# Kernel optimization log

Hardware: AMD Instinct MI355X
Metric: run time of the kernel (lower is better)

Reference implementation:

```python
import jax, jax.numpy as jnp
import numpy as np

B, T, IN, H = 32, 256, 64, 128
TOP_K = 5
TRUNC = 100   # truncate_length: detach h,c every TRUNC steps
EPS = 1e-7
NEG = -1e9


def setup_inputs() -> dict:
    key = jax.random.key(0)
    ks = jax.random.split(key, 6)
    s = 1.0 / np.sqrt(H)  # torch LSTMCell default init bound
    xav = float(1.414 * np.sqrt(6.0 / (2 * H + 1)))  # xavier_uniform gain=1.414
    return {
        "x": jax.random.normal(ks[0], (B, T, IN), jnp.float32),
        "W_ih": jax.random.uniform(ks[1], (4 * H, IN), jnp.float32, -s, s),
        "W_hh": jax.random.uniform(ks[2], (4 * H, H), jnp.float32, -s, s),
        "b_ih": jax.random.uniform(ks[3], (4 * H,), jnp.float32, -s, s),
        "b_hh": jax.random.uniform(ks[4], (4 * H,), jnp.float32, -s, s),
        "w_t": jax.random.uniform(ks[5], (2 * H, 1), jnp.float32, -xav, xav),
    }


def _lstm_cell(x_t, h, c, W_ih, W_hh, b_ih, b_hh):
    # torch gate order: i, f, g, o
    g = x_t @ W_ih.T + h @ W_hh.T + (b_ih + b_hh)
    i, f, gg, o = jnp.split(g, 4, axis=-1)
    c = jax.nn.sigmoid(f) * c + jax.nn.sigmoid(i) * jnp.tanh(gg)
    h = jax.nn.sigmoid(o) * jnp.tanh(c)
    return h, c


def reference(x, W_ih, W_hh, b_ih, b_hh, w_t):
    Bv, Tv, _ = x.shape
    Hh = W_hh.shape[1]
    # score = w_t . tanh(cat(h_t, h_old)) splits additively since tanh is elementwise
    w_a = w_t[:Hh, 0]
    w_b = w_t[Hh:, 0]
    pos = jnp.arange(Tv + 1)

    def step(carry, inp):
        h, c, h_old = carry          # h_old: [B, T+1, H], slot 0 = initial zeros
        i, x_t = inp
        det = ((i + 1) % TRUNC) == 0
        h = jnp.where(det, jax.lax.stop_gradient(h), h)
        c = jnp.where(det, jax.lax.stop_gradient(c), c)
        h, c = _lstm_cell(x_t, h, c, W_ih, W_hh, b_ih, b_hh)
        rem = i + 1                  # remember_size
        mask = pos < rem             # [T+1] valid memory slots
        # attention scores over stored states
        s = (jnp.tanh(h) @ w_a)[:, None] + jnp.tanh(h_old) @ w_b  # [B, T+1]
        s_valid = jnp.where(mask[None, :], s, NEG)
        delta = jax.lax.top_k(s_valid, TOP_K)[0][:, -1] + EPS
        w_sp = jnp.clip(s_valid - delta[:, None], 0.0)
        w_sp = w_sp / (w_sp.sum(axis=1, keepdims=True) + EPS)
        # Sparse_attention returns raw scores when remember_size <= top_k
        attn_w = jnp.where(rem <= TOP_K, s, w_sp)
        attn_c = jnp.einsum('bt,bth->bh', jnp.where(mask[None, :], attn_w, 0.0), h_old)
        h = h + attn_c
        h_old = jax.lax.dynamic_update_slice(h_old, h[:, None, :], (0, rem, 0))
        return (h, c, h_old), (attn_c, attn_w)

    h0 = jnp.zeros((Bv, Hh), x.dtype)
    c0 = jnp.zeros((Bv, Hh), x.dtype)
    buf0 = jnp.zeros((Bv, Tv + 1, Hh), x.dtype)
    xs = (jnp.arange(Tv), jnp.swapaxes(x, 0, 1))
    _, (attn_c_all, attn_w_all) = jax.lax.scan(step, (h0, c0, buf0), xs)
    # module returns last step's (attn_c, out_attn_w); final remember_size == T
    return attn_c_all[-1], attn_w_all[-1][:, :Tv, None]
```

## Files before the change

### kernel.cpp

```cpp
#include <hip/hip_runtime.h>
#include <math.h>

#define NEGF -1000000000.0f
#define EPSF 1e-7f


#define RAWBAR() asm volatile("s_waitcnt lgkmcnt(0)\n\ts_barrier" ::: "memory")

__device__ __forceinline__ float fsigmoid(float x) {
  return 1.0f / (1.0f + __expf(-x));
}
__device__ __forceinline__ float ftanh(float x) {
  return 1.0f - 2.0f / (1.0f + __expf(2.0f * x));
}

__device__ __forceinline__ float wave_allsum(float v) {
#if __has_builtin(__builtin_amdgcn_update_dpp) && __has_builtin(__builtin_amdgcn_readlane)
  float f = v;
#define DPPSTEP(ctrl, rmask) { \
    int t = __builtin_amdgcn_update_dpp(0, __builtin_bit_cast(int, f), \
                                        ctrl, rmask, 0xf, true); \
    f += __builtin_bit_cast(float, t); }
  DPPSTEP(0x111, 0xf)
  DPPSTEP(0x112, 0xf)
  DPPSTEP(0x114, 0xf)
  DPPSTEP(0x118, 0xf)
  DPPSTEP(0x142, 0xa)
  DPPSTEP(0x143, 0x8)
#undef DPPSTEP
  return __builtin_bit_cast(float,
      __builtin_amdgcn_readlane(__builtin_bit_cast(int, f), 63));
#else
  for (int off = 1; off < 64; off <<= 1) v += __shfl_xor(v, off, 64);
  return v;
#endif
}

__global__ __launch_bounds__(512) void xw_kernel(
    const float* __restrict__ x, const float* __restrict__ W_ih,
    const float* __restrict__ b_ih, const float* __restrict__ b_hh,
    float* __restrict__ xw)
{
  const int t0 = blockIdx.x * 32;
  const int b  = blockIdx.y;
  const int g  = threadIdx.x;

  __shared__ float sx[32 * 64];
  ((float4*)sx)[threadIdx.x] =
      ((const float4*)(x + (size_t)(b * 256 + t0) * 64))[threadIdx.x];

  const float4* wr = (const float4*)(W_ih + (size_t)g * 64);
  float4 w0 = wr[0],  w1 = wr[1],  w2 = wr[2],  w3 = wr[3],
         w4 = wr[4],  w5 = wr[5],  w6 = wr[6],  w7 = wr[7],
         w8 = wr[8],  w9 = wr[9],  w10 = wr[10], w11 = wr[11],
         w12 = wr[12], w13 = wr[13], w14 = wr[14], w15 = wr[15];
  const float bias = b_ih[g] + b_hh[g];
  __syncthreads();

  float* dst = xw + (size_t)(b * 256 + t0) * 512 + g;
  for (int tt = 0; tt < 32; ++tt) {
    const float4* xr = (const float4*)(sx + tt * 64);
    float a0 = 0.0f, a1 = 0.0f, a2 = 0.0f, a3 = 0.0f;
#define XSTEP(j) { float4 hv = xr[j]; \
    a0 = fmaf(w##j.x, hv.x, a0); a1 = fmaf(w##j.y, hv.y, a1); \
    a2 = fmaf(w##j.z, hv.z, a2); a3 = fmaf(w##j.w, hv.w, a3); }
    XSTEP(0) XSTEP(1) XSTEP(2) XSTEP(3) XSTEP(4) XSTEP(5) XSTEP(6) XSTEP(7)
    XSTEP(8) XSTEP(9) XSTEP(10) XSTEP(11) XSTEP(12) XSTEP(13) XSTEP(14) XSTEP(15)
#undef XSTEP
    dst[(size_t)tt * 512] = (a0 + a1) + (a2 + a3) + bias;
  }
}

__global__
__attribute__((amdgpu_flat_work_group_size(512, 512), amdgpu_waves_per_eu(2, 2)))
void lstm_attn(
    const float* __restrict__ xw, const float* __restrict__ W_hh,
    const float* __restrict__ w_t, float* __restrict__ out)
{
  const int b   = blockIdx.x;
  const int tid = threadIdx.x;
  const int l   = tid & 63;
  const int wid = tid >> 6;
  const int p   = tid & 127;
  const int q   = tid >> 7;

  __shared__ float ho[257 * 128];
  __shared__ float sh_part[4 * 512];
  __shared__ float sh_d[8];

  const float4* pI = (const float4*)(W_hh + (size_t)(p      ) * 128 + (q << 5));
  const float4* pF = (const float4*)(W_hh + (size_t)(p + 128) * 128 + (q << 5));
  const float4* pG = (const float4*)(W_hh + (size_t)(p + 256) * 128 + (q << 5));
  const float4* pO = (const float4*)(W_hh + (size_t)(p + 384) * 128 + (q << 5));
  float4 wI0 = pI[0], wI1 = pI[1], wI2 = pI[2], wI3 = pI[3],
         wI4 = pI[4], wI5 = pI[5], wI6 = pI[6], wI7 = pI[7];
  float4 wF0 = pF[0], wF1 = pF[1], wF2 = pF[2], wF3 = pF[3],
         wF4 = pF[4], wF5 = pF[5], wF6 = pF[6], wF7 = pF[7];
  float4 wG0 = pG[0], wG1 = pG[1], wG2 = pG[2], wG3 = pG[3],
         wG4 = pG[4], wG5 = pG[5], wG6 = pG[6], wG7 = pG[7];
  float4 wO0 = pO[0], wO1 = pO[1], wO2 = pO[2], wO3 = pO[3],
         wO4 = pO[4], wO5 = pO[5], wO6 = pO[6], wO7 = pO[7];

  const int j0 = 2 * l, j1 = 2 * l + 1;
  float c0 = 0.0f, c1 = 0.0f;
  float wa0 = 0.0f, wa1 = 0.0f, wb0 = 0.0f, wb1 = 0.0f;
  float t5v0 = 0.0f, t5v1 = NEGF, t5v2 = NEGF, t5v3 = NEGF, t5v4 = NEGF;
  int   t5i0 = 0, t5i1 = 0, t5i2 = 0, t5i3 = 0;
  float gn0 = 0.0f, gn1 = 0.0f, gn2 = 0.0f, gn3 = 0.0f;
  int   ofs0 = 0, ofs1 = 0, ofs2 = 0, ofs3 = 0;

  if (wid == 0) {
    wa0 = w_t[j0];       wa1 = w_t[j1];
    wb0 = w_t[128 + j0]; wb1 = w_t[128 + j1];
    *(float2*)(ho + j0) = make_float2(0.0f, 0.0f);
    __builtin_amdgcn_s_setprio(1);
  }
  if (tid == 0) sh_d[0] = 0.0f;
  __syncthreads();

  const float* xwb = xw + (size_t)b * 256 * 512;
  float xcI = 0.0f, xcF = 0.0f, xcG = 0.0f, xcO = 0.0f;
  if (q == 0) {
    xcI = xwb[p];       xcF = xwb[p + 128];
    xcG = xwb[p + 256]; xcO = xwb[p + 384];
  }

  for (int i = 0; i < 256; ++i) {
    const int rem = i + 1;
    float hn0 = 0.0f, hn1 = 0.0f;

    float aI = xcI, aF = xcF, aG = xcG, aO = xcO;
    if (q == 0 && i < 255) {
      const float* xn = xwb + (size_t)(i + 1) * 512;
      xcI = xn[p];       xcF = xn[p + 128];
      xcG = xn[p + 256]; xcO = xn[p + 384];
    }
    const float4* hh4 = (const float4*)(ho + i * 128 + (q << 5));
#define KS(k) { float4 hv = hh4[k]; \
    aI = fmaf(wI##k.x, hv.x, aI); aI = fmaf(wI##k.y, hv.y, aI); \
    aI = fmaf(wI##k.z, hv.z, aI); aI = fmaf(wI##k.w, hv.w, aI); \
    aF = fmaf(wF##k.x, hv.x, aF); aF = fmaf(wF##k.y, hv.y, aF); \
    aF = fmaf(wF##k.z, hv.z, aF); aF = fmaf(wF##k.w, hv.w, aF); \
    aG = fmaf(wG##k.x, hv.x, aG); aG = fmaf(wG##k.y, hv.y, aG); \
    aG = fmaf(wG##k.z, hv.z, aG); aG = fmaf(wG##k.w, hv.w, aG); \
    aO = fmaf(wO##k.x, hv.x, aO); aO = fmaf(wO##k.y, hv.y, aO); \
    aO = fmaf(wO##k.z, hv.z, aO); aO = fmaf(wO##k.w, hv.w, aO); }
    KS(0) KS(1) KS(2) KS(3) KS(4) KS(5) KS(6) KS(7)
#undef KS
    {
      float* sp = sh_part + (q << 9) + p;
      sp[0]   = aI;
      sp[128] = aF;
      sp[256] = aG;
      sp[384] = aO;
    }

    float2 hv0, hv1, hv2, hv3;
    if (wid == 0 && i >= 5) {
      hv0 = *(const float2*)(ho + ofs0);
      hv1 = *(const float2*)(ho + ofs1);
      hv2 = *(const float2*)(ho + ofs2);
      hv3 = *(const float2*)(ho + ofs3);
    }
    RAWBAR();

    if (wid == 0) {
#define GSUM(base) ({ \
      float2 x0 = ((const float2*)(sh_part        + (base)))[l]; \
      float2 x1 = ((const float2*)(sh_part +  512 + (base)))[l]; \
      float2 x2 = ((const float2*)(sh_part + 1024 + (base)))[l]; \
      float2 x3 = ((const float2*)(sh_part + 1536 + (base)))[l]; \
      float2 r; r.x = (x0.x + x1.x) + (x2.x + x3.x); \
      r.y = (x0.y + x1.y) + (x2.y + x3.y); r; })
      float2 Pi = GSUM(0), Pf = GSUM(128), Pg = GSUM(256), Po = GSUM(384);
#undef GSUM
      c0 = fsigmoid(Pf.x) * c0 + fsigmoid(Pi.x) * ftanh(Pg.x);
      c1 = fsigmoid(Pf.y) * c1 + fsigmoid(Pi.y) * ftanh(Pg.y);
      float hc0 = fsigmoid(Po.x) * ftanh(c0);
      float hc1 = fsigmoid(Po.y) * ftanh(c1);

      float at0, at1;
      if (i >= 5) {
        at0 = gn0 * hv0.x;            at1 = gn0 * hv0.y;
        at0 = fmaf(gn1, hv1.x, at0);  at1 = fmaf(gn1, hv1.y, at1);
        at0 = fmaf(gn2, hv2.x, at0);  at1 = fmaf(gn2, hv2.y, at1);
        at0 = fmaf(gn3, hv3.x, at0);  at1 = fmaf(gn3, hv3.y, at1);
      } else {
        float a = wave_allsum(ftanh(hc0) * wa0 + ftanh(hc1) * wa1);
        at0 = 0.0f; at1 = 0.0f;
        for (int t = 0; t <= i; ++t) {
          float s = a + sh_d[t];
          float2 hv = *(const float2*)(ho + t * 128 + j0);
          at0 = fmaf(s, hv.x, at0);
          at1 = fmaf(s, hv.y, at1);
        }
      }
      hn0 = hc0 + at0; hn1 = hc1 + at1;
      *(float2*)(ho + rem * 128 + j0) = make_float2(hn0, hn1);
      if (i == 255) {
        out[b * 128 + j0] = at0; out[b * 128 + j1] = at1;
        #pragma unroll
        for (int m = 0; m < 4; ++m) {
          int t = l + 64 * m;
          float val = 0.0f;
          if (t == t5i0) val = gn0;
          if (t == t5i1) val = gn1;
          if (t == t5i2) val = gn2;
          if (t == t5i3) val = gn3;
          out[4096 + b * 256 + t] = val;
        }
      }
    }
    RAWBAR();

    if (wid == 0 && i < 255) {
      float dn = wave_allsum(ftanh(hn0) * wb0 + ftanh(hn1) * wb1);
      if (l == 0 && i < 4) sh_d[rem] = dn;
      float v = dn; int vi = rem;
      if (v > t5v0) { float tv = t5v0; int ti = t5i0; t5v0 = v; t5i0 = vi; v = tv; vi = ti; }
      if (v > t5v1) { float tv = t5v1; int ti = t5i1; t5v1 = v; t5i1 = vi; v = tv; vi = ti; }
      if (v > t5v2) { float tv = t5v2; int ti = t5i2; t5v2 = v; t5i2 = vi; v = tv; vi = ti; }
      if (v > t5v3) { float tv = t5v3; int ti = t5i3; t5v3 = v; t5i3 = vi; v = tv; vi = ti; }
      if (v > t5v4) { t5v4 = v; }
      float g0 = fmaxf(t5v0 - t5v4 - EPSF, 0.0f);
      float g1 = fmaxf(t5v1 - t5v4 - EPSF, 0.0f);
      float g2 = fmaxf(t5v2 - t5v4 - EPSF, 0.0f);
      float g3 = fmaxf(t5v3 - t5v4 - EPSF, 0.0f);
      float inv = 1.0f / (((g0 + g1) + (g2 + g3)) + EPSF);
      gn0 = g0 * inv; gn1 = g1 * inv; gn2 = g2 * inv; gn3 = g3 * inv;
      ofs0 = (t5i0 << 7) + j0; ofs1 = (t5i1 << 7) + j0;
      ofs2 = (t5i2 << 7) + j0; ofs3 = (t5i3 << 7) + j0;
    }
  }
}

extern "C" void kernel_launch(void* const* d_in, const int* in_sizes, int n_in,
                              void* d_out, int out_size, void* d_ws, size_t ws_size,
                              hipStream_t stream) {
  const float* x    = (const float*)d_in[0];
  const float* W_ih = (const float*)d_in[1];
  const float* W_hh = (const float*)d_in[2];
  const float* b_ih = (const float*)d_in[3];
  const float* b_hh = (const float*)d_in[4];
  const float* w_t  = (const float*)d_in[5];
  float* out = (float*)d_out;

  float* xw = (float*)d_ws;

  xw_kernel<<<dim3(8, 32), 512, 0, stream>>>(x, W_ih, b_ih, b_hh, xw);
  lstm_attn<<<dim3(32), 512, 0, stream>>>(xw, W_hh, w_t, out);
}
```

Before: 398.1 us.

## Fuse input projection into recurrent LSTM kernel with prefetched x ring buffer

Removes the separate xw_kernel and its workspace round trip. The recurrent kernel now keeps W_ih slices in registers and computes the x·W_ih^T contribution each step from a small shared-memory ring of x rows. Wave 7 prefetches those rows several steps ahead. This saves a kernel launch and the global reads of the precomputed projection, but adds 64 FMAs per gate per thread and more register pressure to the serial per-step critical path.

Result: slower. 487.6 us (+22.5%).

```diff
diff --git a/kernel.cpp b/kernel.cpp
--- a/kernel.cpp
+++ b/kernel.cpp
@@ -36,46 +36,13 @@
 #endif
 }
 
-__global__ __launch_bounds__(512) void xw_kernel(
-    const float* __restrict__ x, const float* __restrict__ W_ih,
-    const float* __restrict__ b_ih, const float* __restrict__ b_hh,
-    float* __restrict__ xw)
-{
-  const int t0 = blockIdx.x * 32;
-  const int b  = blockIdx.y;
-  const int g  = threadIdx.x;
-
-  __shared__ float sx[32 * 64];
-  ((float4*)sx)[threadIdx.x] =
-      ((const float4*)(x + (size_t)(b * 256 + t0) * 64))[threadIdx.x];
-
-  const float4* wr = (const float4*)(W_ih + (size_t)g * 64);
-  float4 w0 = wr[0],  w1 = wr[1],  w2 = wr[2],  w3 = wr[3],
-         w4 = wr[4],  w5 = wr[5],  w6 = wr[6],  w7 = wr[7],
-         w8 = wr[8],  w9 = wr[9],  w10 = wr[10], w11 = wr[11],
-         w12 = wr[12], w13 = wr[13], w14 = wr[14], w15 = wr[15];
-  const float bias = b_ih[g] + b_hh[g];
-  __syncthreads();
-
-  float* dst = xw + (size_t)(b * 256 + t0) * 512 + g;
-  for (int tt = 0; tt < 32; ++tt) {
-    const float4* xr = (const float4*)(sx + tt * 64);
-    float a0 = 0.0f, a1 = 0.0f, a2 = 0.0f, a3 = 0.0f;
-#define XSTEP(j) { float4 hv = xr[j]; \
-    a0 = fmaf(w##j.x, hv.x, a0); a1 = fmaf(w##j.y, hv.y, a1); \
-    a2 = fmaf(w##j.z, hv.z, a2); a3 = fmaf(w##j.w, hv.w, a3); }
-    XSTEP(0) XSTEP(1) XSTEP(2) XSTEP(3) XSTEP(4) XSTEP(5) XSTEP(6) XSTEP(7)
-    XSTEP(8) XSTEP(9) XSTEP(10) XSTEP(11) XSTEP(12) XSTEP(13) XSTEP(14) XSTEP(15)
-#undef XSTEP
-    dst[(size_t)tt * 512] = (a0 + a1) + (a2 + a3) + bias;
-  }
-}
-
 __global__
 __attribute__((amdgpu_flat_work_group_size(512, 512), amdgpu_waves_per_eu(2, 2)))
 void lstm_attn(
-    const float* __restrict__ xw, const float* __restrict__ W_hh,
-    const float* __restrict__ w_t, float* __restrict__ out)
+    const float* __restrict__ x, const float* __restrict__ W_ih,
+    const float* __restrict__ W_hh, const float* __restrict__ b_ih,
+    const float* __restrict__ b_hh, const float* __restrict__ w_t,
+    float* __restrict__ out)
 {
   const int b   = blockIdx.x;
   const int tid = threadIdx.x;
@@ -86,6 +53,7 @@
 
   __shared__ float ho[257 * 128];
   __shared__ float sh_part[4 * 512];
+  __shared__ float sxr[8][64];
   __shared__ float sh_d[8];
 
   const float4* pI = (const float4*)(W_hh + (size_t)(p      ) * 128 + (q << 5));
@@ -100,6 +68,20 @@
          wG4 = pG[4], wG5 = pG[5], wG6 = pG[6], wG7 = pG[7];
   float4 wO0 = pO[0], wO1 = pO[1], wO2 = pO[2], wO3 = pO[3],
          wO4 = pO[4], wO5 = pO[5], wO6 = pO[6], wO7 = pO[7];
+  const float4* xI = (const float4*)(W_ih + (size_t)(p      ) * 64 + (q << 4));
+  const float4* xF = (const float4*)(W_ih + (size_t)(p + 128) * 64 + (q << 4));
+  const float4* xG = (const float4*)(W_ih + (size_t)(p + 256) * 64 + (q << 4));
+  const float4* xO = (const float4*)(W_ih + (size_t)(p + 384) * 64 + (q << 4));
+  float4 vI0 = xI[0], vI1 = xI[1], vI2 = xI[2], vI3 = xI[3];
+  float4 vF0 = xF[0], vF1 = xF[1], vF2 = xF[2], vF3 = xF[3];
+  float4 vG0 = xG[0], vG1 = xG[1], vG2 = xG[2], vG3 = xG[3];
+  float4 vO0 = xO[0], vO1 = xO[1], vO2 = xO[2], vO3 = xO[3];
+  const float biasI = (q == 0) ? b_ih[p      ] + b_hh[p      ] : 0.0f;
+  const float biasF = (q == 0) ? b_ih[p + 128] + b_hh[p + 128] : 0.0f;
+  const float biasG = (q == 0) ? b_ih[p + 256] + b_hh[p + 256] : 0.0f;
+  const float biasO = (q == 0) ? b_ih[p + 384] + b_hh[p + 384] : 0.0f;
+
+  const float* xg = x + (size_t)b * 256 * 64;
 
   const int j0 = 2 * l, j1 = 2 * l + 1;
   float c0 = 0.0f, c1 = 0.0f;
@@ -115,26 +97,36 @@
     *(float2*)(ho + j0) = make_float2(0.0f, 0.0f);
     __builtin_amdgcn_s_setprio(1);
   }
+  if (wid == 7) {
+    sxr[0][l] = xg[l];
+    sxr[1][l] = xg[64 + l];
+    sxr[2][l] = xg[128 + l];
+    sxr[3][l] = xg[192 + l];
+    sxr[4][l] = xg[256 + l];
+  }
   if (tid == 0) sh_d[0] = 0.0f;
   __syncthreads();
-
-  const float* xwb = xw + (size_t)b * 256 * 512;
-  float xcI = 0.0f, xcF = 0.0f, xcG = 0.0f, xcO = 0.0f;
-  if (q == 0) {
-    xcI = xwb[p];       xcF = xwb[p + 128];
-    xcG = xwb[p + 256]; xcO = xwb[p + 384];
-  }
 
   for (int i = 0; i < 256; ++i) {
     const int rem = i + 1;
     float hn0 = 0.0f, hn1 = 0.0f;
 
-    float aI = xcI, aF = xcF, aG = xcG, aO = xcO;
-    if (q == 0 && i < 255) {
-      const float* xn = xwb + (size_t)(i + 1) * 512;
-      xcI = xn[p];       xcF = xn[p + 128];
-      xcG = xn[p + 256]; xcO = xn[p + 384];
-    }
+    float xnv = 0.0f;
+    if (wid == 7 && i < 251) xnv = xg[(size_t)(i + 5) * 64 + l];
+
+    float aI = biasI, aF = biasF, aG = biasG, aO = biasO;
+    const float4* xx4 = (const float4*)(&sxr[i & 7][q << 4]);
+#define XS(k) { float4 xv = xx4[k]; \
+    aI = fmaf(vI##k.x, xv.x, aI); aI = fmaf(vI##k.y, xv.y, aI); \
+    aI = fmaf(vI##k.z, xv.z, aI); aI = fmaf(vI##k.w, xv.w, aI); \
+    aF = fmaf(vF##k.x, xv.x, aF); aF = fmaf(vF##k.y, xv.y, aF); \
+    aF = fmaf(vF##k.z, xv.z, aF); aF = fmaf(vF##k.w, xv.w, aF); \
+    aG = fmaf(vG##k.x, xv.x, aG); aG = fmaf(vG##k.y, xv.y, aG); \
+    aG = fmaf(vG##k.z, xv.z, aG); aG = fmaf(vG##k.w, xv.w, aG); \
+    aO = fmaf(vO##k.x, xv.x, aO); aO = fmaf(vO##k.y, xv.y, aO); \
+    aO = fmaf(vO##k.z, xv.z, aO); aO = fmaf(vO##k.w, xv.w, aO); }
+    XS(0) XS(1) XS(2) XS(3)
+#undef XS
     const float4* hh4 = (const float4*)(ho + i * 128 + (q << 5));
 #define KS(k) { float4 hv = hh4[k]; \
     aI = fmaf(wI##k.x, hv.x, aI); aI = fmaf(wI##k.y, hv.y, aI); \
@@ -210,6 +202,8 @@
           out[4096 + b * 256 + t] = val;
         }
       }
+    } else if (wid == 7 && i < 251) {
+      sxr[(i + 5) & 7][l] = xnv;
     }
     RAWBAR();
 
@@ -245,8 +239,6 @@
   const float* w_t  = (const float*)d_in[5];
   float* out = (float*)d_out;
 
-  float* xw = (float*)d_ws;
-
-  xw_kernel<<<dim3(8, 32), 512, 0, stream>>>(x, W_ih, b_ih, b_hh, xw);
-  lstm_attn<<<dim3(32), 512, 0, stream>>>(xw, W_hh, w_t, out);
-}
+  (void)d_ws; (void)ws_size;
+  lstm_attn<<<dim3(32), 512, 0, stream>>>(x, W_ih, W_hh, b_ih, b_hh, w_t, out);
+}
```

## Split LSTM cell update across two waves and vectorize gate FMAs

Applied to the files above, without the earlier changes.

The serial per-step cell update, attention and score reduction move from one wave handling two hidden units per lane to two waves handling one unit each. Partial wave sums are exchanged through shared memory. The recurrent matvec now uses 4-wide vector FMAs with separate accumulators that are summed at the end, which breaks the serial FMA dependency chain. The trade-off is extra cross-wave communication in every step, and an additional barrier in the first five steps.

Result: faster. 367.5 us (-7.7%).

```diff
diff --git a/kernel.cpp b/kernel.cpp
--- a/kernel.cpp
+++ b/kernel.cpp
@@ -4,6 +4,9 @@
 #define NEGF -1000000000.0f
 #define EPSF 1e-7f
 
+
+typedef float v4f __attribute__((ext_vector_type(4)));
+#define FMA4(a, b, c) __builtin_elementwise_fma((a), (b), (c))
 
 #define RAWBAR() asm volatile("s_waitcnt lgkmcnt(0)\n\ts_barrier" ::: "memory")
 
@@ -87,32 +90,33 @@
   __shared__ float ho[257 * 128];
   __shared__ float sh_part[4 * 512];
   __shared__ float sh_d[8];
-
-  const float4* pI = (const float4*)(W_hh + (size_t)(p      ) * 128 + (q << 5));
-  const float4* pF = (const float4*)(W_hh + (size_t)(p + 128) * 128 + (q << 5));
-  const float4* pG = (const float4*)(W_hh + (size_t)(p + 256) * 128 + (q << 5));
-  const float4* pO = (const float4*)(W_hh + (size_t)(p + 384) * 128 + (q << 5));
-  float4 wI0 = pI[0], wI1 = pI[1], wI2 = pI[2], wI3 = pI[3],
-         wI4 = pI[4], wI5 = pI[5], wI6 = pI[6], wI7 = pI[7];
-  float4 wF0 = pF[0], wF1 = pF[1], wF2 = pF[2], wF3 = pF[3],
-         wF4 = pF[4], wF5 = pF[5], wF6 = pF[6], wF7 = pF[7];
-  float4 wG0 = pG[0], wG1 = pG[1], wG2 = pG[2], wG3 = pG[3],
-         wG4 = pG[4], wG5 = pG[5], wG6 = pG[6], wG7 = pG[7];
-  float4 wO0 = pO[0], wO1 = pO[1], wO2 = pO[2], wO3 = pO[3],
-         wO4 = pO[4], wO5 = pO[5], wO6 = pO[6], wO7 = pO[7];
-
-  const int j0 = 2 * l, j1 = 2 * l + 1;
-  float c0 = 0.0f, c1 = 0.0f;
-  float wa0 = 0.0f, wa1 = 0.0f, wb0 = 0.0f, wb1 = 0.0f;
+  __shared__ float sh_pa[2];
+  __shared__ float sh_dn[2];
+
+  const v4f* pI = (const v4f*)(W_hh + (size_t)(p      ) * 128 + (q << 5));
+  const v4f* pF = (const v4f*)(W_hh + (size_t)(p + 128) * 128 + (q << 5));
+  const v4f* pG = (const v4f*)(W_hh + (size_t)(p + 256) * 128 + (q << 5));
+  const v4f* pO = (const v4f*)(W_hh + (size_t)(p + 384) * 128 + (q << 5));
+  v4f wI0 = pI[0], wI1 = pI[1], wI2 = pI[2], wI3 = pI[3],
+      wI4 = pI[4], wI5 = pI[5], wI6 = pI[6], wI7 = pI[7];
+  v4f wF0 = pF[0], wF1 = pF[1], wF2 = pF[2], wF3 = pF[3],
+      wF4 = pF[4], wF5 = pF[5], wF6 = pF[6], wF7 = pF[7];
+  v4f wG0 = pG[0], wG1 = pG[1], wG2 = pG[2], wG3 = pG[3],
+      wG4 = pG[4], wG5 = pG[5], wG6 = pG[6], wG7 = pG[7];
+  v4f wO0 = pO[0], wO1 = pO[1], wO2 = pO[2], wO3 = pO[3],
+      wO4 = pO[4], wO5 = pO[5], wO6 = pO[6], wO7 = pO[7];
+
+  const int j = (wid << 6) + l;
+  float cc = 0.0f;
+  float wa = 0.0f, wb = 0.0f;
   float t5v0 = 0.0f, t5v1 = NEGF, t5v2 = NEGF, t5v3 = NEGF, t5v4 = NEGF;
   int   t5i0 = 0, t5i1 = 0, t5i2 = 0, t5i3 = 0;
   float gn0 = 0.0f, gn1 = 0.0f, gn2 = 0.0f, gn3 = 0.0f;
   int   ofs0 = 0, ofs1 = 0, ofs2 = 0, ofs3 = 0;
 
-  if (wid == 0) {
-    wa0 = w_t[j0];       wa1 = w_t[j1];
-    wb0 = w_t[128 + j0]; wb1 = w_t[128 + j1];
-    *(float2*)(ho + j0) = make_float2(0.0f, 0.0f);
+  if (wid < 2) {
+    wa = w_t[j]; wb = w_t[128 + j];
+    ho[j] = 0.0f;
     __builtin_amdgcn_s_setprio(1);
   }
   if (tid == 0) sh_d[0] = 0.0f;
@@ -127,95 +131,90 @@
 
   for (int i = 0; i < 256; ++i) {
     const int rem = i + 1;
-    float hn0 = 0.0f, hn1 = 0.0f;
-
-    float aI = xcI, aF = xcF, aG = xcG, aO = xcO;
+
+    v4f aI = {xcI, 0.0f, 0.0f, 0.0f};
+    v4f aF = {xcF, 0.0f, 0.0f, 0.0f};
+    v4f aG = {xcG, 0.0f, 0.0f, 0.0f};
+    v4f aO = {xcO, 0.0f, 0.0f, 0.0f};
     if (q == 0 && i < 255) {
       const float* xn = xwb + (size_t)(i + 1) * 512;
       xcI = xn[p];       xcF = xn[p + 128];
       xcG = xn[p + 256]; xcO = xn[p + 384];
     }
-    const float4* hh4 = (const float4*)(ho + i * 128 + (q << 5));
-#define KS(k) { float4 hv = hh4[k]; \
-    aI = fmaf(wI##k.x, hv.x, aI); aI = fmaf(wI##k.y, hv.y, aI); \
-    aI = fmaf(wI##k.z, hv.z, aI); aI = fmaf(wI##k.w, hv.w, aI); \
-    aF = fmaf(wF##k.x, hv.x, aF); aF = fmaf(wF##k.y, hv.y, aF); \
-    aF = fmaf(wF##k.z, hv.z, aF); aF = fmaf(wF##k.w, hv.w, aF); \
-    aG = fmaf(wG##k.x, hv.x, aG); aG = fmaf(wG##k.y, hv.y, aG); \
-    aG = fmaf(wG##k.z, hv.z, aG); aG = fmaf(wG##k.w, hv.w, aG); \
-    aO = fmaf(wO##k.x, hv.x, aO); aO = fmaf(wO##k.y, hv.y, aO); \
-    aO = fmaf(wO##k.z, hv.z, aO); aO = fmaf(wO##k.w, hv.w, aO); }
+    const v4f* hh4 = (const v4f*)(ho + i * 128 + (q << 5));
+#define KS(k) { v4f hv = hh4[k]; \
+    aI = FMA4(wI##k, hv, aI); aF = FMA4(wF##k, hv, aF); \
+    aG = FMA4(wG##k, hv, aG); aO = FMA4(wO##k, hv, aO); }
     KS(0) KS(1) KS(2) KS(3) KS(4) KS(5) KS(6) KS(7)
 #undef KS
     {
       float* sp = sh_part + (q << 9) + p;
-      sp[0]   = aI;
-      sp[128] = aF;
-      sp[256] = aG;
-      sp[384] = aO;
-    }
-
-    float2 hv0, hv1, hv2, hv3;
-    if (wid == 0 && i >= 5) {
-      hv0 = *(const float2*)(ho + ofs0);
-      hv1 = *(const float2*)(ho + ofs1);
-      hv2 = *(const float2*)(ho + ofs2);
-      hv3 = *(const float2*)(ho + ofs3);
+      sp[0]   = (aI.x + aI.y) + (aI.z + aI.w);
+      sp[128] = (aF.x + aF.y) + (aF.z + aF.w);
+      sp[256] = (aG.x + aG.y) + (aG.z + aG.w);
+      sp[384] = (aO.x + aO.y) + (aO.z + aO.w);
+    }
+
+    float hv0 = 0.0f, hv1 = 0.0f, hv2 = 0.0f, hv3 = 0.0f;
+    if (wid < 2 && i >= 5) {
+      hv0 = ho[ofs0]; hv1 = ho[ofs1]; hv2 = ho[ofs2]; hv3 = ho[ofs3];
     }
     RAWBAR();
 
-    if (wid == 0) {
-#define GSUM(base) ({ \
-      float2 x0 = ((const float2*)(sh_part        + (base)))[l]; \
-      float2 x1 = ((const float2*)(sh_part +  512 + (base)))[l]; \
-      float2 x2 = ((const float2*)(sh_part + 1024 + (base)))[l]; \
-      float2 x3 = ((const float2*)(sh_part + 1536 + (base)))[l]; \
-      float2 r; r.x = (x0.x + x1.x) + (x2.x + x3.x); \
-      r.y = (x0.y + x1.y) + (x2.y + x3.y); r; })
-      float2 Pi = GSUM(0), Pf = GSUM(128), Pg = GSUM(256), Po = GSUM(384);
-#undef GSUM
-      c0 = fsigmoid(Pf.x) * c0 + fsigmoid(Pi.x) * ftanh(Pg.x);
-      c1 = fsigmoid(Pf.y) * c1 + fsigmoid(Pi.y) * ftanh(Pg.y);
-      float hc0 = fsigmoid(Po.x) * ftanh(c0);
-      float hc1 = fsigmoid(Po.y) * ftanh(c1);
-
-      float at0, at1;
-      if (i >= 5) {
-        at0 = gn0 * hv0.x;            at1 = gn0 * hv0.y;
-        at0 = fmaf(gn1, hv1.x, at0);  at1 = fmaf(gn1, hv1.y, at1);
-        at0 = fmaf(gn2, hv2.x, at0);  at1 = fmaf(gn2, hv2.y, at1);
-        at0 = fmaf(gn3, hv3.x, at0);  at1 = fmaf(gn3, hv3.y, at1);
-      } else {
-        float a = wave_allsum(ftanh(hc0) * wa0 + ftanh(hc1) * wa1);
-        at0 = 0.0f; at1 = 0.0f;
-        for (int t = 0; t <= i; ++t) {
-          float s = a + sh_d[t];
-          float2 hv = *(const float2*)(ho + t * 128 + j0);
-          at0 = fmaf(s, hv.x, at0);
-          at1 = fmaf(s, hv.y, at1);
+    float hc = 0.0f, at = 0.0f;
+    if (wid < 2) {
+      const float* s0 = sh_part + j;
+      float Pi = (s0[0]         + s0[512])         + (s0[1024]         + s0[1536]);
+      float Pf = (s0[128]       + s0[640])         + (s0[1152]         + s0[1664]);
+      float Pg = (s0[256]       + s0[768])         + (s0[1280]         + s0[1792]);
+      float Po = (s0[384]       + s0[896])         + (s0[1408]         + s0[1920]);
+      cc = fsigmoid(Pf) * cc + fsigmoid(Pi) * ftanh(Pg);
+      hc = fsigmoid(Po) * ftanh(cc);
+    }
+    if (i < 5) {
+      if (wid < 2) {
+        float pa = wave_allsum(ftanh(hc) * wa);
+        if (l == 0) sh_pa[wid] = pa;
+      }
+      RAWBAR();
+      if (wid < 2) {
+        float a = sh_pa[0] + sh_pa[1];
+        at = 0.0f;
+        for (int t = 0; t <= i; ++t)
+          at = fmaf(a + sh_d[t], ho[t * 128 + j], at);
+      }
+    } else if (wid < 2) {
+      at = gn0 * hv0;
+      at = fmaf(gn1, hv1, at);
+      at = fmaf(gn2, hv2, at);
+      at = fmaf(gn3, hv3, at);
+    }
+    if (wid < 2) {
+      float hn = hc + at;
+      ho[rem * 128 + j] = hn;
+      float pdn = wave_allsum(ftanh(hn) * wb);
+      if (l == 0) sh_dn[wid] = pdn;
+      if (i == 255) {
+        out[b * 128 + j] = at;
+        if (wid == 0) {
+          #pragma unroll
+          for (int m = 0; m < 4; ++m) {
+            int t = l + 64 * m;
+            float val = 0.0f;
+            if (t == t5i0) val = gn0;
+            if (t == t5i1) val = gn1;
+            if (t == t5i2) val = gn2;
+            if (t == t5i3) val = gn3;
+            out[4096 + b * 256 + t] = val;
+          }
         }
       }
-      hn0 = hc0 + at0; hn1 = hc1 + at1;
-      *(float2*)(ho + rem * 128 + j0) = make_float2(hn0, hn1);
-      if (i == 255) {
-        out[b * 128 + j0] = at0; out[b * 128 + j1] = at1;
-        #pragma unroll
-        for (int m = 0; m < 4; ++m) {
-          int t = l + 64 * m;
-          float val = 0.0f;
-          if (t == t5i0) val = gn0;
-          if (t == t5i1) val = gn1;
-          if (t == t5i2) val = gn2;
-          if (t == t5i3) val = gn3;
-          out[4096 + b * 256 + t] = val;
-        }
-      }
     }
     RAWBAR();
 
-    if (wid == 0 && i < 255) {
-      float dn = wave_allsum(ftanh(hn0) * wb0 + ftanh(hn1) * wb1);
-      if (l == 0 && i < 4) sh_d[rem] = dn;
+    if (wid < 2 && i < 255) {
+      float dn = sh_dn[0] + sh_dn[1];
+      if (wid == 0 && l == 0 && i < 4) sh_d[rem] = dn;
       float v = dn; int vi = rem;
       if (v > t5v0) { float tv = t5v0; int ti = t5i0; t5v0 = v; t5i0 = vi; v = tv; vi = ti; }
       if (v > t5v1) { float tv = t5v1; int ti = t5i1; t5v1 = v; t5i1 = vi; v = tv; vi = ti; }
@@ -228,8 +227,8 @@
       float g3 = fmaxf(t5v3 - t5v4 - EPSF, 0.0f);
       float inv = 1.0f / (((g0 + g1) + (g2 + g3)) + EPSF);
       gn0 = g0 * inv; gn1 = g1 * inv; gn2 = g2 * inv; gn3 = g3 * inv;
-      ofs0 = (t5i0 << 7) + j0; ofs1 = (t5i1 << 7) + j0;
-      ofs2 = (t5i2 << 7) + j0; ofs3 = (t5i3 << 7) + j0;
+      ofs0 = (t5i0 << 7) + j; ofs1 = (t5i1 << 7) + j;
+      ofs2 = (t5i2 << 7) + j; ofs3 = (t5i3 << 7) + j;
     }
   }
 }
```
